# Kernel optimization log

Measured on AMD Instinct MI355X. Metric: run time of the kernel, lower is better.

## Reference

```python
import jax, jax.numpy as jnp
import numpy as np

D_MODEL, D_STATE, BATCH, SEQ = 512, 32, 8, 4096

def _hippo(n):
    i = np.arange(n)[:, None].astype(np.float64)
    j = np.arange(n)[None, :].astype(np.float64)
    P = np.where(i > j, np.sqrt(2 * i + 1) * np.sqrt(2 * j + 1), 0.0)
    P = P + np.diag(np.arange(1, n + 1).astype(np.float64))
    return (-P).astype(np.float32)

def setup_inputs() -> dict:
    key = jax.random.key(0)
    k0, k1, k2, k3 = jax.random.split(key, 4)
    x = jax.random.normal(k0, (BATCH, SEQ, D_MODEL), dtype=jnp.float32)
    A = jnp.asarray(_hippo(D_STATE))
    B = jax.random.normal(k1, (D_STATE, D_MODEL), dtype=jnp.float32) / np.float32(np.sqrt(D_MODEL))
    C = jax.random.normal(k2, (D_MODEL, D_STATE), dtype=jnp.float32) / np.float32(np.sqrt(D_STATE))
    D = jnp.ones((D_MODEL,), dtype=jnp.float32)
    log_dt = jnp.zeros((D_MODEL,), dtype=jnp.float32)
    W_out = jax.random.normal(k3, (D_MODEL, D_MODEL), dtype=jnp.float32) / np.float32(np.sqrt(D_MODEL))
    b_out = jnp.zeros((D_MODEL,), dtype=jnp.float32)
    return {"x": x, "A": A, "B": B, "C": C, "D": D, "log_dt": log_dt, "W_out": W_out, "b_out": b_out}

def reference(x, A, B, C, D, log_dt, W_out, b_out):
    # x: (b, s, d). S4 layer with bilinear discretization and tanh recurrence.
    n = A.shape[0]
    dt = jnp.mean(jnp.clip(jnp.exp(log_dt), 1e-4, 1.0))  # scalar dt.mean()
    I = jnp.eye(n, dtype=x.dtype)
    inv_term = jnp.linalg.inv(I - 0.5 * dt * A)
    A_bar = (I + 0.5 * dt * A) @ inv_term          # (n, n)
    B_bar = dt * (inv_term @ B)                    # (n, d)
    # Precompute input projection for all timesteps (vectorized):
    uB = jnp.einsum('bsd,nd->bsn', x, B_bar)       # (b, s, n)
    s0 = jnp.zeros((x.shape[0], n), dtype=x.dtype)
    def step(state, ub_t):
        state = jnp.tanh(state @ A_bar.T + ub_t)   # (b, n)
        return state, state
    final_state, states = jax.lax.scan(step, s0, jnp.swapaxes(uB, 0, 1))
    states = jnp.swapaxes(states, 0, 1)            # (b, s, n)
    y = jnp.einsum('bsn,dn->bsd', states, C) + x * D
    y = y @ W_out.T + b_out                        # output_proj (dropout = eval identity)
    return y, final_state
```

## Files before the change

### kernel.cpp

```cpp
#include <hip/hip_runtime.h>
#include <hip/hip_bf16.h>

#define D_MODEL 512
#define D_STATE 32
#define BATCH 8
#define SEQ 4096
#define MROWS (BATCH * SEQ)

typedef __bf16 bf16;
typedef __bf16 bf16x4 __attribute__((ext_vector_type(4)));
typedef __bf16 bf16x8 __attribute__((ext_vector_type(8)));
typedef float f32x4 __attribute__((ext_vector_type(4)));

#define CHUNK 16
#define BURN 80
#define NCHUNK (SEQ / CHUNK)

__device__ __forceinline__ bf16x8 cvt8(const f32x4 a, const f32x4 b) {
  bf16x8 h;
  h[0] = (bf16)a[0]; h[1] = (bf16)a[1]; h[2] = (bf16)a[2]; h[3] = (bf16)a[3];
  h[4] = (bf16)b[0]; h[5] = (bf16)b[1]; h[6] = (bf16)b[2]; h[7] = (bf16)b[3];
  return h;
}

__global__ __launch_bounds__(256) void k_pre(
    const float* __restrict__ A, const float* __restrict__ C, const float* __restrict__ Dv,
    const float* __restrict__ log_dt, const float* __restrict__ W,
    float* __restrict__ A_bar, float* __restrict__ XTs,
    bf16* __restrict__ CW, bf16* __restrict__ WD) {
  __shared__ float Xs[32][32];
  const int bid = blockIdx.x, t = threadIdx.x;
  float* Xf = &Xs[0][0];

  if (bid == 0) {
    {
      float v0 = __expf(log_dt[t]);
      float v1 = __expf(log_dt[t + 256]);
      v0 = fminf(fmaxf(v0, 1e-4f), 1.0f);
      v1 = fminf(fmaxf(v1, 1e-4f), 1.0f);
      Xf[t] = v0 + v1;
    }
    __syncthreads();
    for (int s2 = 128; s2 > 0; s2 >>= 1) {
      if (t < s2) Xf[t] += Xf[t + s2];
      __syncthreads();
    }
    const float dtv = Xf[0] * (1.0f / 512.0f);
    __syncthreads();
    {
      const int i0 = 4 * t;
      const f32x4 av = *(const f32x4*)(A + i0);
      f32x4 mv;
#pragma unroll
      for (int q = 0; q < 4; q++) {
        const int r = (i0 + q) >> 5, c = (i0 + q) & 31;
        mv[q] = (r == c ? 1.0f : 0.0f) - 0.5f * dtv * av[q];
      }
      *(f32x4*)(Xf + i0) = mv;
    }
    __syncthreads();
    if (t < 32) {
      const int j = t;
      float xcol[32];
#pragma unroll
      for (int i = 0; i < 32; i++) {
        float s0 = 0.f, s1 = 0.f, s2 = 0.f, s3 = 0.f;
#pragma unroll
        for (int k = 0; k < 32; k += 4) {
          if (k < i)     s0 -= Xf[i * 32 + k]     * xcol[k];
          if (k + 1 < i) s1 -= Xf[i * 32 + k + 1] * xcol[k + 1];
          if (k + 2 < i) s2 -= Xf[i * 32 + k + 2] * xcol[k + 2];
          if (k + 3 < i) s3 -= Xf[i * 32 + k + 3] * xcol[k + 3];
        }
        const float num = (i == j ? 1.0f : 0.0f) + ((s0 + s1) + (s2 + s3));
        xcol[i] = (i >= j) ? num / Xf[i * 32 + i] : 0.0f;
      }
#pragma unroll
      for (int i = 0; i < 32; i++) Xs[i][j] = xcol[i];
    }
    __syncthreads();
    {
      const int i0 = 4 * t;
      const int r = t >> 3;
      f32x4 ov;
#pragma unroll
      for (int q = 0; q < 4; q++) {
        const int c = (i0 + q) & 31;
        float s = 0.f;
#pragma unroll
        for (int k = 0; k < 32; k++) {
          const float p2 = (r == k ? 1.0f : 0.0f) + 0.5f * dtv * A[r * 32 + k];
          s = fmaf(p2, Xf[k * 32 + c], s);
        }
        ov[q] = s;
      }
      *(f32x4*)(A_bar + i0) = ov;
    }
#pragma unroll
    for (int i = 0; i < 4; i++) {
      const int idx = t + i * 256;
      const int k = idx >> 5, n = idx & 31;
      XTs[idx] = dtv * Xf[n * 32 + k];
    }
  } else if (bid <= 16) {
    const int w = t >> 6, lane = t & 63;
    const int l15 = lane & 15, kg = lane >> 4;
    const int m = w & 1, nf = w >> 1;
    const int eb = (bid - 1) * 32;
    const float* wp = W + (long)(eb + m * 16 + l15) * D_MODEL + kg * 8;
    const int ncol = nf * 16 + l15;
    f32x4 acc = (f32x4)(0.0f);
#pragma unroll 1
    for (int kt = 0; kt < 16; kt++) {
      const f32x4 w0 = *(const f32x4*)(wp + kt * 32);
      const f32x4 w1 = *(const f32x4*)(wp + kt * 32 + 4);
      const bf16x8 af = cvt8(w0, w1);
      bf16x8 bf;
#pragma unroll
      for (int j = 0; j < 8; j++)
        bf[j] = (bf16)C[(kt * 32 + kg * 8 + j) * D_STATE + ncol];
      acc = __builtin_amdgcn_mfma_f32_16x16x32_bf16(af, bf, acc, 0, 0, 0);
    }
#pragma unroll
    for (int jj = 0; jj < 4; jj++)
      CW[(eb + m * 16 + kg * 4 + jj) * D_STATE + ncol] = (bf16)acc[jj];
  } else {
#pragma unroll
    for (int jj = 0; jj < 16; jj++) {
      const int i = (bid - 17) * 16384 + jj * 1024 + t * 4;
      const f32x4 wv = *(const f32x4*)(W + i);
      const f32x4 dv = *(const f32x4*)(Dv + (i & 511));
      bf16x4 h;
#pragma unroll
      for (int q = 0; q < 4; q++) h[q] = (bf16)(wv[q] * dv[q]);
      *(bf16x4*)(WD + i) = h;
    }
  }
}

__global__ __launch_bounds__(256, 2) void k_uB(
    const float* __restrict__ x, const float* __restrict__ B,
    const float* __restrict__ XTs,
    float* __restrict__ uB, bf16* __restrict__ xb) {
  __shared__ float sXT[1024];
  __shared__ float srw[64 * 33];
  const int t = threadIdx.x, w = t >> 6, lane = t & 63;
  const int l15 = lane & 15, kg = lane >> 4;
  const long rowbase = (long)blockIdx.x * 64;

#pragma unroll
  for (int i = 0; i < 4; i++) sXT[t + i * 256] = XTs[t + i * 256];

  const int arow = w * 16 + l15;
  const float* xp = x + (rowbase + arow) * D_MODEL + kg * 8;
  bf16* xo = xb + (rowbase + arow) * D_MODEL + kg * 8;
  const float* bp0 = B + l15 * D_MODEL + kg * 8;
  const float* bp1 = B + (16 + l15) * D_MODEL + kg * 8;

  f32x4 acc0 = (f32x4)(0.0f), acc1 = (f32x4)(0.0f);
  f32x4 cx0, cx1, cb00, cb01, cb10, cb11;
  f32x4 nx0, nx1, nb00, nb01, nb10, nb11;
  cx0 = *(const f32x4*)(xp);      cx1 = *(const f32x4*)(xp + 4);
  cb00 = *(const f32x4*)(bp0);    cb01 = *(const f32x4*)(bp0 + 4);
  cb10 = *(const f32x4*)(bp1);    cb11 = *(const f32x4*)(bp1 + 4);

#pragma unroll 1
  for (int kt = 0; kt < 16; kt++) {
    if (kt < 15) {
      const int o = (kt + 1) * 32;
      nx0 = *(const f32x4*)(xp + o);    nx1 = *(const f32x4*)(xp + o + 4);
      nb00 = *(const f32x4*)(bp0 + o);  nb01 = *(const f32x4*)(bp0 + o + 4);
      nb10 = *(const f32x4*)(bp1 + o);  nb11 = *(const f32x4*)(bp1 + o + 4);
    }
    const bf16x8 af = cvt8(cx0, cx1);
    *(bf16x8*)(xo + kt * 32) = af;
    const bf16x8 bh0 = cvt8(cb00, cb01);
    const bf16x8 bh1 = cvt8(cb10, cb11);
    bf16x8 bl0, bl1;
#pragma unroll
    for (int q = 0; q < 4; q++) {
      bl0[q]     = (bf16)(cb00[q] - (float)bh0[q]);
      bl0[q + 4] = (bf16)(cb01[q] - (float)bh0[q + 4]);
      bl1[q]     = (bf16)(cb10[q] - (float)bh1[q]);
      bl1[q + 4] = (bf16)(cb11[q] - (float)bh1[q + 4]);
    }
    acc0 = __builtin_amdgcn_mfma_f32_16x16x32_bf16(af, bh0, acc0, 0, 0, 0);
    acc0 = __builtin_amdgcn_mfma_f32_16x16x32_bf16(af, bl0, acc0, 0, 0, 0);
    acc1 = __builtin_amdgcn_mfma_f32_16x16x32_bf16(af, bh1, acc1, 0, 0, 0);
    acc1 = __builtin_amdgcn_mfma_f32_16x16x32_bf16(af, bl1, acc1, 0, 0, 0);
    cx0 = nx0; cx1 = nx1;
    cb00 = nb00; cb01 = nb01; cb10 = nb10; cb11 = nb11;
  }
#pragma unroll
  for (int jj = 0; jj < 4; jj++) {
    srw[(w * 16 + kg * 4 + jj) * 33 + l15]      = acc0[jj];
    srw[(w * 16 + kg * 4 + jj) * 33 + 16 + l15] = acc1[jj];
  }
  __syncthreads();
  {
    const int r = t & 63, ng = t >> 6;
    f32x4 u0 = (f32x4)(0.0f), u1 = (f32x4)(0.0f);
#pragma unroll
    for (int k = 0; k < 32; k++) {
      const float sv = srw[r * 33 + k];
      const f32x4 x0 = *(const f32x4*)&sXT[k * 32 + ng * 4];
      const f32x4 x1 = *(const f32x4*)&sXT[k * 32 + ng * 4 + 16];
#pragma unroll
      for (int q = 0; q < 4; q++) {
        u0[q] = fmaf(sv, x0[q], u0[q]);
        u1[q] = fmaf(sv, x1[q], u1[q]);
      }
    }
    float* up = uB + (rowbase + r) * D_STATE;
    *(f32x4*)(up + ng * 4) = u0;
    *(f32x4*)(up + ng * 4 + 16) = u1;
  }
}

__global__ void k_scan(const float* __restrict__ uB, const float* __restrict__ A_bar,
                       bf16* __restrict__ Sb, float* __restrict__ fs) {
  __shared__ float sbuf[256];
  const int t = threadIdx.x;
  const int g = t >> 5, n = t & 31;
  const int chain = blockIdx.x * 8 + g;
  const int b = chain >> 8;
  const int ch = chain & 255;
  const int cs = ch * CHUNK;
  const int t0 = cs - BURN;
  const int ce = cs + CHUNK;

  float a[32];
#pragma unroll
  for (int k = 0; k < 32; k += 4) {
    const f32x4 v = *(const f32x4*)(A_bar + n * 32 + k);
    a[k] = v[0]; a[k + 1] = v[1]; a[k + 2] = v[2]; a[k + 3] = v[3];
  }
#pragma unroll
  for (int k = 0; k < 32; k++) asm volatile("" : "+v"(a[k]));

  const float* ub = uB + (long)b * SEQ * D_STATE + n;
  bf16* sp = Sb + ((long)b * SEQ + cs) * D_STATE + n;
  float* myslot = &sbuf[g * 32];

  float s = 0.f;
  float ubuf[8], unext[8];
#pragma unroll
  for (int i = 0; i < 8; i++) {
    const int tt = t0 + i;
    ubuf[i] = (tt >= 0) ? ub[(long)tt * D_STATE] : 0.f;
  }
  for (int tg = t0; tg < ce; tg += 8) {
    const int tn = tg + 8;
#pragma unroll
    for (int i = 0; i < 8; i++) {
      const int tt = tn + i;
      unext[i] = (tt >= 0 && tt < ce) ? ub[(long)tt * D_STATE] : 0.f;
    }
#pragma unroll
    for (int i = 0; i < 8; i++) {
      const int tt = tg + i;
      myslot[n] = s;
      const f32x4 s0 = *(const f32x4*)(myslot + 0);
      const f32x4 s1 = *(const f32x4*)(myslot + 4);
      const f32x4 s2 = *(const f32x4*)(myslot + 8);
      const f32x4 s3 = *(const f32x4*)(myslot + 12);
      const f32x4 s4 = *(const f32x4*)(myslot + 16);
      const f32x4 s5 = *(const f32x4*)(myslot + 20);
      const f32x4 s6 = *(const f32x4*)(myslot + 24);
      const f32x4 s7 = *(const f32x4*)(myslot + 28);
      float acc0 = ubuf[i], acc1 = 0.f, acc2 = 0.f, acc3 = 0.f;
#pragma unroll
      for (int q = 0; q < 4; q++) {
        acc0 = fmaf(a[0 + q],  s0[q], acc0);
        acc1 = fmaf(a[4 + q],  s1[q], acc1);
        acc2 = fmaf(a[8 + q],  s2[q], acc2);
        acc3 = fmaf(a[12 + q], s3[q], acc3);
        acc0 = fmaf(a[16 + q], s4[q], acc0);
        acc1 = fmaf(a[20 + q], s5[q], acc1);
        acc2 = fmaf(a[24 + q], s6[q], acc2);
        acc3 = fmaf(a[28 + q], s7[q], acc3);
      }
      const float z = (acc0 + acc1) + (acc2 + acc3);
      const float e = __expf(2.f * z);
      const float r = __builtin_amdgcn_rcpf(e + 1.f);
      s = fmaf(-2.f, r, 1.f);
      if (tt >= cs) sp[(long)(tt - cs) * D_STATE] = (bf16)s;
    }
#pragma unroll
    for (int i = 0; i < 8; i++) ubuf[i] = unext[i];
  }
  if (ch == NCHUNK - 1) fs[b * D_STATE + n] = s;
}

__device__ __forceinline__ void stage_tile(const void* gbase, long row0, long rowStrideB,
                                           int kByte, void* lds, int w, int lane) {
#pragma unroll
  for (int j = 0; j < 2; j++) {
    const int base_off = (w << 11) + (j << 10);
    const int boff = base_off + (lane << 4);
    const int r = boff >> 6;
    const int s = (boff >> 4) & 3;
    const int cb = ((s ^ (r & 3)) << 4);
    const char* src = (const char*)gbase + (row0 + r) * rowStrideB + kByte + cb;
    __builtin_amdgcn_global_load_lds(
        (const __attribute__((address_space(1))) void*)src,
        (__attribute__((address_space(3))) void*)((char*)lds + base_off), 16, 0, 0);
  }
}

__global__ __launch_bounds__(256) void k_out(const bf16* __restrict__ xb,
                                             const bf16* __restrict__ WD,
                                             const bf16* __restrict__ Sb,
                                             const bf16* __restrict__ CW,
                                             const float* __restrict__ bias,
                                             float* __restrict__ out) {
  __shared__ bf16 As[2][128 * 32];
  __shared__ bf16 Bs[2][128 * 32];
  const int tid = threadIdx.x;
  const int w = tid >> 6, lane = tid & 63;
  const int swz = (blockIdx.x & 7) * 128 + (blockIdx.x >> 3);
  const int bm = swz >> 2, bn = swz & 3;
  const long rowbase = (long)bm * 128;
  const long colbase = (long)bn * 128;
  const int wr = w >> 1, wc = w & 1;
  const int l15 = lane & 15, kg = lane >> 4;
  const int kgs = kg ^ (l15 & 3);

  f32x4 acc[4][4];
#pragma unroll
  for (int m = 0; m < 4; m++)
#pragma unroll
    for (int n = 0; n < 4; n++) acc[m][n] = (f32x4)(0.0f);

  const int aoff = (wr * 64 + l15) * 32 + kgs * 8;
  const int boff = (wc * 64 + l15) * 32 + kgs * 8;

  auto STAGE = [&](int ti, int b) {
    if (ti < 16) {
      stage_tile(xb, rowbase, 1024, ti * 64, &As[b][0], w, lane);
      stage_tile(WD, colbase, 1024, ti * 64, &Bs[b][0], w, lane);
    } else {
      stage_tile(Sb, rowbase, 64, 0, &As[b][0], w, lane);
      stage_tile(CW, colbase, 64, 0, &Bs[b][0], w, lane);
    }
  };

  STAGE(0, 0);
  __syncthreads();
#pragma unroll 1
  for (int kt = 0; kt < 17; kt++) {
    const int cur = kt & 1;
    if (kt < 16) STAGE(kt + 1, cur ^ 1);
    bf16x8 af[4], bfr[4];
#pragma unroll
    for (int m = 0; m < 4; m++) af[m] = *(const bf16x8*)&As[cur][aoff + m * 16 * 32];
#pragma unroll
    for (int n = 0; n < 4; n++) bfr[n] = *(const bf16x8*)&Bs[cur][boff + n * 16 * 32];
#pragma unroll
    for (int m = 0; m < 4; m++)
#pragma unroll
      for (int n = 0; n < 4; n++)
        acc[m][n] = __builtin_amdgcn_mfma_f32_16x16x32_bf16(af[m], bfr[n], acc[m][n], 0, 0, 0);
    __syncthreads();
  }
#pragma unroll
  for (int n = 0; n < 4; n++) {
    const int e = (int)colbase + wc * 64 + n * 16 + l15;
    const float bv = bias[e];
#pragma unroll
    for (int m = 0; m < 4; m++) {
      const long r0 = rowbase + wr * 64 + m * 16 + kg * 4;
      const f32x4 v = acc[m][n];
#pragma unroll
      for (int jj = 0; jj < 4; jj++) out[(r0 + jj) * (long)D_MODEL + e] = v[jj] + bv;
    }
  }
}

extern "C" void kernel_launch(void* const* d_in, const int* in_sizes, int n_in,
                              void* d_out, int out_size, void* d_ws, size_t ws_size,
                              hipStream_t stream) {
  const float* x      = (const float*)d_in[0];
  const float* A      = (const float*)d_in[1];
  const float* B      = (const float*)d_in[2];
  const float* C      = (const float*)d_in[3];
  const float* Dv     = (const float*)d_in[4];
  const float* log_dt = (const float*)d_in[5];
  const float* W      = (const float*)d_in[6];
  const float* b_out  = (const float*)d_in[7];
  float* out = (float*)d_out;
  float* fs  = out + (long)MROWS * D_MODEL;

  char* ws = (char*)d_ws;
  float* A_bar = (float*)(ws + 0);
  float* XTs   = (float*)(ws + (4L << 10));
  bf16*  CW    = (bf16*)(ws + (68L << 10));
  bf16*  WD    = (bf16*)(ws + (100L << 10));
  bf16*  Sb    = (bf16*)(ws + (612L << 10));
  float* uB    = (float*)(ws + (2660L << 10));
  bf16*  xb    = (bf16*)(ws + (6756L << 10));

  k_pre<<<dim3(33), dim3(256), 0, stream>>>(A, C, Dv, log_dt, W, A_bar, XTs, CW, WD);
  k_uB<<<dim3(MROWS / 64), dim3(256), 0, stream>>>(x, B, XTs, uB, xb);
  k_scan<<<dim3(256), dim3(256), 0, stream>>>(uB, A_bar, Sb, fs);
  k_out<<<dim3((MROWS / 128) * (D_MODEL / 128)), dim3(256), 0, stream>>>(xb, WD, Sb, CW, b_out, out);
}
```

Before: 95.63 us.

## Load GEMM fragments directly to registers and deepen prefetch in uB projection

```diff
diff --git a/kernel.cpp b/kernel.cpp
--- a/kernel.cpp
+++ b/kernel.cpp
@@ -138,6 +138,29 @@
   }
 }
 
+#define LOADST(P, KT) { const int _o = (KT) * 32;                      \
+    P##x0 = *(const f32x4*)(xp + _o);   P##x1 = *(const f32x4*)(xp + _o + 4);  \
+    P##b0 = *(const f32x4*)(bp0 + _o);  P##b1 = *(const f32x4*)(bp0 + _o + 4); \
+    P##b2 = *(const f32x4*)(bp1 + _o);  P##b3 = *(const f32x4*)(bp1 + _o + 4); }
+
+#define COMP(P, KT) {                                                  \
+    const bf16x8 af = cvt8(P##x0, P##x1);                              \
+    *(bf16x8*)(xo + (KT) * 32) = af;                                   \
+    const bf16x8 bh0 = cvt8(P##b0, P##b1);                             \
+    const bf16x8 bh1 = cvt8(P##b2, P##b3);                             \
+    bf16x8 bl0, bl1;                                                   \
+    _Pragma("unroll")                                                  \
+    for (int q = 0; q < 4; q++) {                                      \
+      bl0[q]     = (bf16)(P##b0[q] - (float)bh0[q]);                   \
+      bl0[q + 4] = (bf16)(P##b1[q] - (float)bh0[q + 4]);               \
+      bl1[q]     = (bf16)(P##b2[q] - (float)bh1[q]);                   \
+      bl1[q + 4] = (bf16)(P##b3[q] - (float)bh1[q + 4]);               \
+    }                                                                  \
+    acc0 = __builtin_amdgcn_mfma_f32_16x16x32_bf16(af, bh0, acc0, 0, 0, 0); \
+    acc0 = __builtin_amdgcn_mfma_f32_16x16x32_bf16(af, bl0, acc0, 0, 0, 0); \
+    acc1 = __builtin_amdgcn_mfma_f32_16x16x32_bf16(af, bh1, acc1, 0, 0, 0); \
+    acc1 = __builtin_amdgcn_mfma_f32_16x16x32_bf16(af, bl1, acc1, 0, 0, 0); }
+
 __global__ __launch_bounds__(256, 2) void k_uB(
     const float* __restrict__ x, const float* __restrict__ B,
     const float* __restrict__ XTs,
@@ -158,38 +181,18 @@
   const float* bp1 = B + (16 + l15) * D_MODEL + kg * 8;
 
   f32x4 acc0 = (f32x4)(0.0f), acc1 = (f32x4)(0.0f);
-  f32x4 cx0, cx1, cb00, cb01, cb10, cb11;
-  f32x4 nx0, nx1, nb00, nb01, nb10, nb11;
-  cx0 = *(const f32x4*)(xp);      cx1 = *(const f32x4*)(xp + 4);
-  cb00 = *(const f32x4*)(bp0);    cb01 = *(const f32x4*)(bp0 + 4);
-  cb10 = *(const f32x4*)(bp1);    cb11 = *(const f32x4*)(bp1 + 4);
+  f32x4 P0x0, P0x1, P0b0, P0b1, P0b2, P0b3;
+  f32x4 P1x0, P1x1, P1b0, P1b1, P1b2, P1b3;
+  f32x4 P2x0, P2x1, P2b0, P2b1, P2b2, P2b3;
+  f32x4 P3x0, P3x1, P3b0, P3b1, P3b2, P3b3;
+  LOADST(P0, 0) LOADST(P1, 1) LOADST(P2, 2) LOADST(P3, 3)
 
 #pragma unroll 1
-  for (int kt = 0; kt < 16; kt++) {
-    if (kt < 15) {
-      const int o = (kt + 1) * 32;
-      nx0 = *(const f32x4*)(xp + o);    nx1 = *(const f32x4*)(xp + o + 4);
-      nb00 = *(const f32x4*)(bp0 + o);  nb01 = *(const f32x4*)(bp0 + o + 4);
-      nb10 = *(const f32x4*)(bp1 + o);  nb11 = *(const f32x4*)(bp1 + o + 4);
-    }
-    const bf16x8 af = cvt8(cx0, cx1);
-    *(bf16x8*)(xo + kt * 32) = af;
-    const bf16x8 bh0 = cvt8(cb00, cb01);
-    const bf16x8 bh1 = cvt8(cb10, cb11);
-    bf16x8 bl0, bl1;
-#pragma unroll
-    for (int q = 0; q < 4; q++) {
-      bl0[q]     = (bf16)(cb00[q] - (float)bh0[q]);
-      bl0[q + 4] = (bf16)(cb01[q] - (float)bh0[q + 4]);
-      bl1[q]     = (bf16)(cb10[q] - (float)bh1[q]);
-      bl1[q + 4] = (bf16)(cb11[q] - (float)bh1[q + 4]);
-    }
-    acc0 = __builtin_amdgcn_mfma_f32_16x16x32_bf16(af, bh0, acc0, 0, 0, 0);
-    acc0 = __builtin_amdgcn_mfma_f32_16x16x32_bf16(af, bl0, acc0, 0, 0, 0);
-    acc1 = __builtin_amdgcn_mfma_f32_16x16x32_bf16(af, bh1, acc1, 0, 0, 0);
-    acc1 = __builtin_amdgcn_mfma_f32_16x16x32_bf16(af, bl1, acc1, 0, 0, 0);
-    cx0 = nx0; cx1 = nx1;
-    cb00 = nb00; cb01 = nb01; cb10 = nb10; cb11 = nb11;
+  for (int kt = 0; kt < 16; kt += 4) {
+    COMP(P0, kt)     if (kt + 4 < 16) LOADST(P0, kt + 4)
+    COMP(P1, kt + 1) if (kt + 5 < 16) LOADST(P1, kt + 5)
+    COMP(P2, kt + 2) if (kt + 6 < 16) LOADST(P2, kt + 6)
+    COMP(P3, kt + 3) if (kt + 7 < 16) LOADST(P3, kt + 7)
   }
 #pragma unroll
   for (int jj = 0; jj < 4; jj++) {
@@ -292,21 +295,19 @@
   if (ch == NCHUNK - 1) fs[b * D_STATE + n] = s;
 }
 
-__device__ __forceinline__ void stage_tile(const void* gbase, long row0, long rowStrideB,
-                                           int kByte, void* lds, int w, int lane) {
-#pragma unroll
-  for (int j = 0; j < 2; j++) {
-    const int base_off = (w << 11) + (j << 10);
-    const int boff = base_off + (lane << 4);
-    const int r = boff >> 6;
-    const int s = (boff >> 4) & 3;
-    const int cb = ((s ^ (r & 3)) << 4);
-    const char* src = (const char*)gbase + (row0 + r) * rowStrideB + kByte + cb;
-    __builtin_amdgcn_global_load_lds(
-        (const __attribute__((address_space(1))) void*)src,
-        (__attribute__((address_space(3))) void*)((char*)lds + base_off), 16, 0, 0);
-  }
-}
+#define KO_LOAD(P, KT) {                                               \
+    _Pragma("unroll")                                                  \
+    for (int m = 0; m < 4; m++) {                                      \
+      P##a[m] = *(const bf16x8*)(ap + (KT) * 32 + m * (16 * 512));     \
+      P##b[m] = *(const bf16x8*)(bp + (KT) * 32 + m * (16 * 512));     \
+    } }
+
+#define KO_COMP(P) {                                                   \
+    _Pragma("unroll")                                                  \
+    for (int m = 0; m < 4; m++)                                        \
+      _Pragma("unroll")                                                \
+      for (int n = 0; n < 4; n++)                                      \
+        acc[m][n] = __builtin_amdgcn_mfma_f32_16x16x32_bf16(P##a[m], P##b[n], acc[m][n], 0, 0, 0); }
 
 __global__ __launch_bounds__(256) void k_out(const bf16* __restrict__ xb,
                                              const bf16* __restrict__ WD,
@@ -314,8 +315,6 @@
                                              const bf16* __restrict__ CW,
                                              const float* __restrict__ bias,
                                              float* __restrict__ out) {
-  __shared__ bf16 As[2][128 * 32];
-  __shared__ bf16 Bs[2][128 * 32];
   const int tid = threadIdx.x;
   const int w = tid >> 6, lane = tid & 63;
   const int swz = (blockIdx.x & 7) * 128 + (blockIdx.x >> 3);
@@ -324,7 +323,11 @@
   const long colbase = (long)bn * 128;
   const int wr = w >> 1, wc = w & 1;
   const int l15 = lane & 15, kg = lane >> 4;
-  const int kgs = kg ^ (l15 & 3);
+
+  const bf16* ap = xb + (rowbase + wr * 64 + l15) * 512 + kg * 8;
+  const bf16* bp = WD + (colbase + wc * 64 + l15) * 512 + kg * 8;
+  const bf16* sap = Sb + (rowbase + wr * 64 + l15) * 32 + kg * 8;
+  const bf16* sbp = CW + (colbase + wc * 64 + l15) * 32 + kg * 8;
 
   f32x4 acc[4][4];
 #pragma unroll
@@ -332,37 +335,24 @@
 #pragma unroll
     for (int n = 0; n < 4; n++) acc[m][n] = (f32x4)(0.0f);
 
-  const int aoff = (wr * 64 + l15) * 32 + kgs * 8;
-  const int boff = (wc * 64 + l15) * 32 + kgs * 8;
-
-  auto STAGE = [&](int ti, int b) {
-    if (ti < 16) {
-      stage_tile(xb, rowbase, 1024, ti * 64, &As[b][0], w, lane);
-      stage_tile(WD, colbase, 1024, ti * 64, &Bs[b][0], w, lane);
-    } else {
-      stage_tile(Sb, rowbase, 64, 0, &As[b][0], w, lane);
-      stage_tile(CW, colbase, 64, 0, &Bs[b][0], w, lane);
-    }
-  };
-
-  STAGE(0, 0);
-  __syncthreads();
+  bf16x8 Ta[4], Tb[4];
+#pragma unroll
+  for (int m = 0; m < 4; m++) {
+    Ta[m] = *(const bf16x8*)(sap + m * (16 * 32));
+    Tb[m] = *(const bf16x8*)(sbp + m * (16 * 32));
+  }
+
+  bf16x8 F0a[4], F0b[4], F1a[4], F1b[4];
+  KO_LOAD(F0, 0) KO_LOAD(F1, 1)
 #pragma unroll 1
-  for (int kt = 0; kt < 17; kt++) {
-    const int cur = kt & 1;
-    if (kt < 16) STAGE(kt + 1, cur ^ 1);
-    bf16x8 af[4], bfr[4];
-#pragma unroll
-    for (int m = 0; m < 4; m++) af[m] = *(const bf16x8*)&As[cur][aoff + m * 16 * 32];
-#pragma unroll
-    for (int n = 0; n < 4; n++) bfr[n] = *(const bf16x8*)&Bs[cur][boff + n * 16 * 32];
-#pragma unroll
-    for (int m = 0; m < 4; m++)
-#pragma unroll
-      for (int n = 0; n < 4; n++)
-        acc[m][n] = __builtin_amdgcn_mfma_f32_16x16x32_bf16(af[m], bfr[n], acc[m][n], 0, 0, 0);
-    __syncthreads();
-  }
+  for (int kt = 0; kt < 16; kt += 2) {
+    KO_COMP(F0)
+    if (kt + 2 < 16) KO_LOAD(F0, kt + 2)
+    KO_COMP(F1)
+    if (kt + 3 < 16) KO_LOAD(F1, kt + 3)
+  }
+  KO_COMP(T)
+
 #pragma unroll
   for (int n = 0; n < 4; n++) {
     const int e = (int)colbase + wc * 64 + n * 16 + l15;
```

New measurement: 129.5 us. 1.35x slower.
